# Kernel optimization log

Measured on AMD Instinct MI355X. Metric: run time of the kernel, lower is better.

The kernel has to match this reference:

```python
import jax, jax.numpy as jnp
import numpy as np

B = 16384      # batch
T = 14         # number of embedding tables
L = 100000     # rows per table (table has L+1 rows due to the +1 offset)
E = 16         # em_size
H = 50         # user click history length


def setup_inputs() -> dict:
    key = jax.random.key(0)
    ks = jax.random.split(key, 10)
    sparse_features = jax.random.randint(ks[0], (B, T), 0, L, dtype=jnp.int32)
    dense_features = jax.random.normal(ks[1], (B, 1), dtype=jnp.float32)
    user_click_history = jax.random.randint(ks[2], (B, H), 0, L, dtype=jnp.int32)
    # stacked EmbeddingBag weights: [T, L+1, E]
    W = jax.random.normal(ks[3], (T, L + 1, E), dtype=jnp.float32) * 0.01
    fc1_w = jax.random.normal(ks[4], (200, 241), dtype=jnp.float32) / np.sqrt(241).astype(np.float32)
    fc1_b = jnp.zeros((200,), jnp.float32)
    fc2_w = jax.random.normal(ks[5], (80, 200), dtype=jnp.float32) / np.sqrt(200).astype(np.float32)
    fc2_b = jnp.zeros((80,), jnp.float32)
    fc3_w = jax.random.normal(ks[6], (2, 80), dtype=jnp.float32) / np.sqrt(80).astype(np.float32)
    fc3_b = jnp.zeros((2,), jnp.float32)
    return dict(sparse_features=sparse_features, dense_features=dense_features,
                user_click_history=user_click_history, W=W,
                fc1_w=fc1_w, fc1_b=fc1_b, fc2_w=fc2_w, fc2_b=fc2_b,
                fc3_w=fc3_w, fc3_b=fc3_b)


def reference(sparse_features, dense_features, user_click_history, W,
              fc1_w, fc1_b, fc2_w, fc2_b, fc3_w, fc3_b):
    # Per-table single-index EmbeddingBag(sum) == plain lookup. Batched gather
    # across all T tables at once: [B, T, E]
    embs = W[jnp.arange(T)[None, :], sparse_features + 1]
    embs = embs.reshape(embs.shape[0], T * E)  # [B, T*E]
    # tables[0].weight row 0 is zeroed before the history lookup (padding row).
    W0 = W[0].at[0].set(0.0)
    hist = W0[user_click_history + 1].sum(axis=1)  # [B, E] EmbeddingBag sum
    x = jnp.concatenate([embs, hist, dense_features], axis=1)  # [B, 241]
    x = jax.nn.relu(x @ fc1_w.T + fc1_b)
    x = jax.nn.relu(x @ fc2_w.T + fc2_b)
    return x @ fc3_w.T + fc3_b  # [B, 2]
```

## Files before the change

### kernel.cpp

```cpp
#include <hip/hip_runtime.h>


using u16 = unsigned short;
typedef __attribute__((ext_vector_type(8))) short short8v;
typedef __attribute__((ext_vector_type(4))) float floatx4;

constexpr int BM = 32;
constexpr int NBLK = 16384 / BM;

constexpr int W1_ELEMS = 13 * 8 * 64 * 8;
constexpr int W2_ELEMS = 5 * 7 * 64 * 8;

__device__ __forceinline__ u16 f2bf(float f) {
  unsigned u = __float_as_uint(f);
  unsigned r = (u + 0x7fffu + ((u >> 16) & 1u)) >> 16;
  return (u16)r;
}
__device__ __forceinline__ float bf2f(u16 h) {
  return __uint_as_float(((unsigned)h) << 16);
}

__device__ __forceinline__ void wrA1(u16* Ah, u16* Al, int r, int k, float v) {
  u16 hi = f2bf(v);
  u16 lo = f2bf(v - bf2f(hi));
  int kt = k >> 5, kg = (k >> 3) & 3, e = k & 7;
  int lane = kg * 16 + (r & 15);
  int idx = (((r >> 4) * 8 + kt) * 64 + lane) * 8 + e;
  Ah[idx] = hi;
  Al[idx] = lo;
}

__global__ void build_frags(const float* __restrict__ w1, const float* __restrict__ w2,
                            u16* __restrict__ w1h, u16* __restrict__ w2h) {
  int tid = blockIdx.x * blockDim.x + threadIdx.x;
  if (tid < 13 * 8 * 64) {
    int l = tid & 63;
    int g = tid >> 6;
    int kt = g & 7, nt = g >> 3;
    int n = nt * 16 + (l & 15);
    int kb = kt * 32 + (l >> 4) * 8;
    short8v h8;
#pragma unroll
    for (int e = 0; e < 8; ++e) {
      int k = kb + e;
      float v = (n < 200 && k < 241) ? w1[n * 241 + k] : 0.f;
      h8[e] = (short)f2bf(v);
    }
    *(short8v*)&w1h[tid * 8] = h8;
  } else if (tid < 13 * 8 * 64 + 5 * 7 * 64) {
    int t2 = tid - 13 * 8 * 64;
    int l = t2 & 63;
    int g = t2 >> 6;
    int kt = g % 7, nt = g / 7;
    int n = nt * 16 + (l & 15);
    int kb = kt * 32 + (l >> 4) * 8;
    short8v h8;
#pragma unroll
    for (int e = 0; e < 8; ++e) {
      int k = kb + e;
      float v = (k < 200) ? w2[n * 200 + k] : 0.f;
      h8[e] = (short)f2bf(v);
    }
    *(short8v*)&w2h[t2 * 8] = h8;
  }
}

__global__ __launch_bounds__(1024, 8) void fused_kernel(
    const int* __restrict__ sf, const float* __restrict__ dense,
    const int* __restrict__ hist, const float* __restrict__ W,
    const u16* __restrict__ w1h, const u16* __restrict__ w2h,
    const float* __restrict__ b1, const float* __restrict__ b2,
    const float* __restrict__ w3, const float* __restrict__ b3,
    float* __restrict__ out) {
  __shared__ u16 sm[16384];
  __shared__ float psum[32 * 68];
  const int tid = threadIdx.x;
  const int row0 = blockIdx.x * BM;
  const int l = tid & 63;
  const int wv = tid >> 6;
  const int rh = wv & 1;
  const int pg = wv >> 1;

  short8v z8 = {0, 0, 0, 0, 0, 0, 0, 0};

  short8v bhr[2];
#pragma unroll
  for (int s = 0; s < 2; ++s) {
    int nt = pg + 8 * s;
    bhr[s] = (nt < 13) ? *(const short8v*)&w1h[((nt * 8 + 0) * 64 + l) * 8] : z8;
  }

#pragma unroll
  for (int i = 0; i < 2; ++i) *(short8v*)&sm[(tid + i * 1024) * 8] = z8;
  __syncthreads();

  u16* A1h = sm;
  u16* A1l = sm + 8192;

  if (tid < 512) {
    int r = tid >> 4, rem = tid & 15, q = rem >> 2, s = rem & 3;
    int rg = row0 + r;
    int beg = s * 12 + (s < 2 ? s : 2);
    int cnt = 12 + (s < 2 ? 1 : 0);
    float a0 = 0.f, a1 = 0.f, a2 = 0.f, a3 = 0.f;
    const int* hp = hist + rg * 50;
#pragma unroll 4
    for (int h = beg; h < beg + cnt; ++h) {
      int idx = hp[h] + 1;
      const float* p = W + (size_t)idx * 16 + q * 4;
      a0 += p[0];
      a1 += p[1];
      a2 += p[2];
      a3 += p[3];
    }
    float* ps = &psum[r * 68 + (q * 4) * 4 + s];
    ps[0] = a0;
    ps[4] = a1;
    ps[8] = a2;
    ps[12] = a3;
  } else {
    int tid2 = tid - 512;
#pragma unroll
    for (int it = 0; it < 4; ++it) {
      int g = tid2 + it * 512;
      if (g < 1792) {
        int q = g & 3, rt = g >> 2;
        int r = rt & 31, t = rt >> 5;
        int rg = row0 + r;
        int idx = sf[rg * 14 + t] + 1;
        const float* p = W + ((size_t)t * 100001 + (size_t)idx) * 16 + q * 4;
        float v0 = p[0], v1 = p[1], v2 = p[2], v3 = p[3];
        int kb = t * 16 + q * 4;
        wrA1(A1h, A1l, r, kb + 0, v0);
        wrA1(A1h, A1l, r, kb + 1, v1);
        wrA1(A1h, A1l, r, kb + 2, v2);
        wrA1(A1h, A1l, r, kb + 3, v3);
      }
    }
  }
  __syncthreads();

  if (tid < 512) {
    int r = tid >> 4, d = tid & 15;
    const float* ps = &psum[r * 68 + d * 4];
    float v = ps[0] + ps[1] + ps[2] + ps[3];
    wrA1(A1h, A1l, r, 224 + d, v);
    if (d == 0) wrA1(A1h, A1l, r, 240, dense[row0 + r]);
  }
  __syncthreads();

  floatx4 acc[2];
#pragma unroll
  for (int i = 0; i < 2; ++i) acc[i] = (floatx4){0.f, 0.f, 0.f, 0.f};

#pragma unroll
  for (int kt = 0; kt < 8; ++kt) {
    short8v ah = *(const short8v*)&A1h[((rh * 8 + kt) * 64 + l) * 8];
    short8v al = *(const short8v*)&A1l[((rh * 8 + kt) * 64 + l) * 8];
#pragma unroll
    for (int j = 0; j < 2; ++j) {
      int f = kt * 2 + j;
      int nt = pg + 8 * j;
      short8v cbh = bhr[j];
      int f2 = f + 2;
      if (f2 < 16) {
        int nt2 = pg + 8 * (f2 & 1);
        int kt2 = f2 >> 1;
        if (nt2 < 13) bhr[j] = *(const short8v*)&w1h[((nt2 * 8 + kt2) * 64 + l) * 8];
      }
      if (nt < 13) {
        acc[j] = __builtin_amdgcn_mfma_f32_16x16x32_bf16(ah, cbh, acc[j], 0, 0, 0);
        acc[j] = __builtin_amdgcn_mfma_f32_16x16x32_bf16(al, cbh, acc[j], 0, 0, 0);
      }
    }
  }
  __syncthreads();

#pragma unroll
  for (int i = 0; i < 2; ++i) {
    int b = tid + i * 1024;
    if (b < 1792) *(short8v*)&sm[b * 8] = z8;
  }
  __syncthreads();

  u16* A2h = sm;
  u16* A2l = sm + 7168;

#pragma unroll
  for (int j = 0; j < 2; ++j) {
    int nt = pg + 8 * j;
    if (nt < 13) {
      int n = nt * 16 + (l & 15);
      if (n < 200) {
        float bias = b1[n];
#pragma unroll
        for (int rg_ = 0; rg_ < 4; ++rg_) {
          float v = fmaxf(acc[j][rg_] + bias, 0.f);
          int m = (l >> 4) * 4 + rg_;
          u16 hi = f2bf(v);
          u16 lo = f2bf(v - bf2f(hi));
          int kt = n >> 5, kg = (n >> 3) & 3, e = n & 7;
          int lane2 = kg * 16 + m;
          int idx = ((rh * 7 + kt) * 64 + lane2) * 8 + e;
          A2h[idx] = hi;
          A2l[idx] = lo;
        }
      }
    }
  }
  __syncthreads();

  floatx4 acc2 = (floatx4){0.f, 0.f, 0.f, 0.f};
  if (pg < 5) {
    short8v b2hr[2];
    b2hr[0] = *(const short8v*)&w2h[((pg * 7 + 0) * 64 + l) * 8];
    b2hr[1] = *(const short8v*)&w2h[((pg * 7 + 1) * 64 + l) * 8];
#pragma unroll
    for (int kt = 0; kt < 7; ++kt) {
      short8v ah = *(const short8v*)&A2h[((rh * 7 + kt) * 64 + l) * 8];
      short8v al = *(const short8v*)&A2l[((rh * 7 + kt) * 64 + l) * 8];
      short8v cb = b2hr[kt & 1];
      if (kt + 2 < 7) b2hr[kt & 1] = *(const short8v*)&w2h[((pg * 7 + kt + 2) * 64 + l) * 8];
      acc2 = __builtin_amdgcn_mfma_f32_16x16x32_bf16(ah, cb, acc2, 0, 0, 0);
      acc2 = __builtin_amdgcn_mfma_f32_16x16x32_bf16(al, cb, acc2, 0, 0, 0);
    }
  }
  __syncthreads();

  float* o2 = (float*)sm;
  if (pg < 5) {
    int n = pg * 16 + (l & 15);
    float bias = b2[n];
#pragma unroll
    for (int rg_ = 0; rg_ < 4; ++rg_) {
      int r = rh * 16 + (l >> 4) * 4 + rg_;
      float v = fmaxf(acc2[rg_] + bias, 0.f);
      o2[r * 81 + n] = v;
    }
  }
  __syncthreads();

  if (tid < 64) {
    int r = tid >> 1, o = tid & 1;
    float a = b3[o];
#pragma unroll 8
    for (int j = 0; j < 80; ++j) a += o2[r * 81 + j] * w3[o * 80 + j];
    out[(row0 + r) * 2 + o] = a;
  }
}

extern "C" void kernel_launch(void* const* d_in, const int* in_sizes, int n_in,
                              void* d_out, int out_size, void* d_ws, size_t ws_size,
                              hipStream_t stream) {
  const int* sf = (const int*)d_in[0];
  const float* dense = (const float*)d_in[1];
  const int* hist = (const int*)d_in[2];
  const float* W = (const float*)d_in[3];
  const float* w1 = (const float*)d_in[4];
  const float* b1 = (const float*)d_in[5];
  const float* w2 = (const float*)d_in[6];
  const float* b2 = (const float*)d_in[7];
  const float* w3 = (const float*)d_in[8];
  const float* b3 = (const float*)d_in[9];
  float* out = (float*)d_out;

  u16* w1h = (u16*)d_ws;
  u16* w2h = w1h + W1_ELEMS;

  build_frags<<<dim3(35), dim3(256), 0, stream>>>(w1, w2, w1h, w2h);
  fused_kernel<<<dim3(NBLK), dim3(1024), 0, stream>>>(sf, dense, hist, W, w1h, w2h,
                                                      b1, b2, w3, b3, out);
}
```

Measured before the change: 30.92 us.

## Shrink blocks to 16 rows and 4 waves, redistribute MFMA tiles per wave

Each block now handles 16 batch rows with 256 threads instead of 32 rows with 1024 threads, launching 1024 blocks. Each wave now computes several fc1 and fc2 N-tiles rather than one or two. The history sum is reduced with lane shuffles instead of a shared-memory partial-sum pass, and embedding fragments are written as packed 4-element vectors. Several zero-fill passes and barriers are removed. The aim is better occupancy and latency hiding for the gather-heavy work and fewer synchronisations, at the cost of reloading the weight fragments for every 16 rows instead of every 32.

```diff
diff --git a/kernel.cpp b/kernel.cpp
--- a/kernel.cpp
+++ b/kernel.cpp
@@ -3,10 +3,8 @@
 
 using u16 = unsigned short;
 typedef __attribute__((ext_vector_type(8))) short short8v;
+typedef __attribute__((ext_vector_type(4))) short short4v;
 typedef __attribute__((ext_vector_type(4))) float floatx4;
-
-constexpr int BM = 32;
-constexpr int NBLK = 16384 / BM;
 
 constexpr int W1_ELEMS = 13 * 8 * 64 * 8;
 constexpr int W2_ELEMS = 5 * 7 * 64 * 8;
@@ -18,16 +16,6 @@
 }
 __device__ __forceinline__ float bf2f(u16 h) {
   return __uint_as_float(((unsigned)h) << 16);
-}
-
-__device__ __forceinline__ void wrA1(u16* Ah, u16* Al, int r, int k, float v) {
-  u16 hi = f2bf(v);
-  u16 lo = f2bf(v - bf2f(hi));
-  int kt = k >> 5, kg = (k >> 3) & 3, e = k & 7;
-  int lane = kg * 16 + (r & 15);
-  int idx = (((r >> 4) * 8 + kt) * 64 + lane) * 8 + e;
-  Ah[idx] = hi;
-  Al[idx] = lo;
 }
 
 __global__ void build_frags(const float* __restrict__ w1, const float* __restrict__ w2,
@@ -65,186 +53,218 @@
   }
 }
 
-__global__ __launch_bounds__(1024, 8) void fused_kernel(
+__global__ __launch_bounds__(256, 4) void fused_kernel(
     const int* __restrict__ sf, const float* __restrict__ dense,
     const int* __restrict__ hist, const float* __restrict__ W,
     const u16* __restrict__ w1h, const u16* __restrict__ w2h,
     const float* __restrict__ b1, const float* __restrict__ b2,
     const float* __restrict__ w3, const float* __restrict__ b3,
     float* __restrict__ out) {
-  __shared__ u16 sm[16384];
-  __shared__ float psum[32 * 68];
+  __shared__ u16 A1h[8 * 64 * 8], A1l[8 * 64 * 8];
+  __shared__ u16 A2h[7 * 64 * 8], A2l[7 * 64 * 8];
+  __shared__ float o2[16 * 84];
+
   const int tid = threadIdx.x;
-  const int row0 = blockIdx.x * BM;
   const int l = tid & 63;
   const int wv = tid >> 6;
-  const int rh = wv & 1;
-  const int pg = wv >> 1;
-
+  const int row0 = blockIdx.x * 16;
   short8v z8 = {0, 0, 0, 0, 0, 0, 0, 0};
 
-  short8v bhr[2];
-#pragma unroll
-  for (int s = 0; s < 2; ++s) {
-    int nt = pg + 8 * s;
-    bhr[s] = (nt < 13) ? *(const short8v*)&w1h[((nt * 8 + 0) * 64 + l) * 8] : z8;
-  }
-
-#pragma unroll
-  for (int i = 0; i < 2; ++i) *(short8v*)&sm[(tid + i * 1024) * 8] = z8;
-  __syncthreads();
-
-  u16* A1h = sm;
-  u16* A1l = sm + 8192;
-
-  if (tid < 512) {
-    int r = tid >> 4, rem = tid & 15, q = rem >> 2, s = rem & 3;
-    int rg = row0 + r;
-    int beg = s * 12 + (s < 2 ? s : 2);
-    int cnt = 12 + (s < 2 ? 1 : 0);
+  const int ntbase = (wv == 0) ? 0 : 4 + 3 * (wv - 1);
+  const int ntcnt = (wv == 0) ? 4 : 3;
+
+  short8v bhr[2][4];
+#pragma unroll
+  for (int kk = 0; kk < 2; ++kk)
+#pragma unroll
+    for (int i = 0; i < 4; ++i)
+      bhr[kk][i] = (i < ntcnt) ? *(const short8v*)&w1h[(((ntbase + i) * 8 + kk) * 64 + l) * 8]
+                               : z8;
+
+#pragma unroll
+  for (int it = 0; it < 4; ++it) {
+    int g = tid + it * 256;
+    if (g < 896) {
+      int q = g & 3, rt = g >> 2;
+      int r = rt & 15, t = rt >> 4;
+      int idx = sf[(row0 + r) * 14 + t] + 1;
+      const float* p = W + ((size_t)t * 100001 + (size_t)idx) * 16 + q * 4;
+      int k0 = t * 16 + q * 4;
+      int kt = k0 >> 5, kg = (k0 >> 3) & 3, e0 = k0 & 7;
+      short4v h4, l4;
+#pragma unroll
+      for (int d = 0; d < 4; ++d) {
+        float v = p[d];
+        u16 hi = f2bf(v);
+        h4[d] = (short)hi;
+        l4[d] = (short)f2bf(v - bf2f(hi));
+      }
+      int base = (kt * 64 + kg * 16 + r) * 8 + e0;
+      *(short4v*)&A1h[base] = h4;
+      *(short4v*)&A1l[base] = l4;
+    }
+  }
+
+  {
+    int r = tid >> 4, rem = tid & 15, q = rem & 3, s = rem >> 2;
+    const int* hp = hist + (row0 + r) * 50;
+    const float* Wq = W + q * 4;
     float a0 = 0.f, a1 = 0.f, a2 = 0.f, a3 = 0.f;
-    const int* hp = hist + rg * 50;
-#pragma unroll 4
-    for (int h = beg; h < beg + cnt; ++h) {
-      int idx = hp[h] + 1;
-      const float* p = W + (size_t)idx * 16 + q * 4;
+#pragma unroll
+    for (int hh = 0; hh < 12; ++hh) {
+      int idx = hp[s + hh * 4] + 1;
+      const float* p = Wq + (size_t)idx * 16;
       a0 += p[0];
       a1 += p[1];
       a2 += p[2];
       a3 += p[3];
     }
-    float* ps = &psum[r * 68 + (q * 4) * 4 + s];
-    ps[0] = a0;
-    ps[4] = a1;
-    ps[8] = a2;
-    ps[12] = a3;
+    if (s < 2) {
+      int idx = hp[48 + s] + 1;
+      const float* p = Wq + (size_t)idx * 16;
+      a0 += p[0];
+      a1 += p[1];
+      a2 += p[2];
+      a3 += p[3];
+    }
+    a0 += __shfl_xor(a0, 4);
+    a1 += __shfl_xor(a1, 4);
+    a2 += __shfl_xor(a2, 4);
+    a3 += __shfl_xor(a3, 4);
+    a0 += __shfl_xor(a0, 8);
+    a1 += __shfl_xor(a1, 8);
+    a2 += __shfl_xor(a2, 8);
+    a3 += __shfl_xor(a3, 8);
+    if (s == 0) {
+      float vals[4] = {a0, a1, a2, a3};
+      short4v h4, l4;
+#pragma unroll
+      for (int d = 0; d < 4; ++d) {
+        u16 hi = f2bf(vals[d]);
+        h4[d] = (short)hi;
+        l4[d] = (short)f2bf(vals[d] - bf2f(hi));
+      }
+      int base = (7 * 64 + (q >> 1) * 16 + r) * 8 + ((q * 4) & 7);
+      *(short4v*)&A1h[base] = h4;
+      *(short4v*)&A1l[base] = l4;
+      if (q == 0) {
+        float dv = dense[row0 + r];
+        u16 dh = f2bf(dv), dl = f2bf(dv - bf2f(dh));
+        short8v dh8 = z8, dl8 = z8;
+        dh8[0] = (short)dh;
+        dl8[0] = (short)dl;
+        *(short8v*)&A1h[(7 * 64 + 32 + r) * 8] = dh8;
+        *(short8v*)&A1l[(7 * 64 + 32 + r) * 8] = dl8;
+        *(short8v*)&A1h[(7 * 64 + 48 + r) * 8] = z8;
+        *(short8v*)&A1l[(7 * 64 + 48 + r) * 8] = z8;
+      }
+    }
+  }
+  __syncthreads();
+
+  floatx4 acc[4];
+#pragma unroll
+  for (int i = 0; i < 4; ++i) acc[i] = (floatx4){0.f, 0.f, 0.f, 0.f};
+
+#pragma unroll
+  for (int kt = 0; kt < 8; ++kt) {
+    short8v ah = *(const short8v*)&A1h[(kt * 64 + l) * 8];
+    short8v al = *(const short8v*)&A1l[(kt * 64 + l) * 8];
+#pragma unroll
+    for (int i = 0; i < 4; ++i) {
+      if (i < ntcnt) {
+        short8v cb = bhr[kt & 1][i];
+        if (kt < 6) bhr[kt & 1][i] = *(const short8v*)&w1h[(((ntbase + i) * 8 + kt + 2) * 64 + l) * 8];
+        acc[i] = __builtin_amdgcn_mfma_f32_16x16x32_bf16(ah, cb, acc[i], 0, 0, 0);
+        acc[i] = __builtin_amdgcn_mfma_f32_16x16x32_bf16(al, cb, acc[i], 0, 0, 0);
+      }
+    }
+  }
+
+  const int ntA = wv;
+  short8v bra[2], brb[2];
+  bra[0] = *(const short8v*)&w2h[((ntA * 7 + 0) * 64 + l) * 8];
+  bra[1] = *(const short8v*)&w2h[((ntA * 7 + 1) * 64 + l) * 8];
+  if (wv == 0) {
+    brb[0] = *(const short8v*)&w2h[((4 * 7 + 0) * 64 + l) * 8];
+    brb[1] = *(const short8v*)&w2h[((4 * 7 + 1) * 64 + l) * 8];
   } else {
-    int tid2 = tid - 512;
-#pragma unroll
-    for (int it = 0; it < 4; ++it) {
-      int g = tid2 + it * 512;
-      if (g < 1792) {
-        int q = g & 3, rt = g >> 2;
-        int r = rt & 31, t = rt >> 5;
-        int rg = row0 + r;
-        int idx = sf[rg * 14 + t] + 1;
-        const float* p = W + ((size_t)t * 100001 + (size_t)idx) * 16 + q * 4;
-        float v0 = p[0], v1 = p[1], v2 = p[2], v3 = p[3];
-        int kb = t * 16 + q * 4;
-        wrA1(A1h, A1l, r, kb + 0, v0);
-        wrA1(A1h, A1l, r, kb + 1, v1);
-        wrA1(A1h, A1l, r, kb + 2, v2);
-        wrA1(A1h, A1l, r, kb + 3, v3);
-      }
-    }
+    brb[0] = z8;
+    brb[1] = z8;
+  }
+
+#pragma unroll
+  for (int i = 0; i < 4; ++i) {
+    if (i < ntcnt) {
+      int n = (ntbase + i) * 16 + (l & 15);
+      float bias = (n < 200) ? b1[n] : 0.f;
+#pragma unroll
+      for (int g = 0; g < 4; ++g) {
+        float v = (n < 200) ? fmaxf(acc[i][g] + bias, 0.f) : 0.f;
+        int m = (l >> 4) * 4 + g;
+        u16 hi = f2bf(v), lo = f2bf(v - bf2f(hi));
+        int kt2 = n >> 5, kg2 = (n >> 3) & 3, e = n & 7;
+        int pos = (kt2 * 64 + kg2 * 16 + m) * 8 + e;
+        A2h[pos] = hi;
+        A2l[pos] = lo;
+      }
+    }
+  }
+  if (wv == 1 && l < 32) {
+    *(short8v*)&A2h[(6 * 64 + 32 + l) * 8] = z8;
+    *(short8v*)&A2l[(6 * 64 + 32 + l) * 8] = z8;
   }
   __syncthreads();
 
-  if (tid < 512) {
-    int r = tid >> 4, d = tid & 15;
-    const float* ps = &psum[r * 68 + d * 4];
-    float v = ps[0] + ps[1] + ps[2] + ps[3];
-    wrA1(A1h, A1l, r, 224 + d, v);
-    if (d == 0) wrA1(A1h, A1l, r, 240, dense[row0 + r]);
+  floatx4 acca = (floatx4){0.f, 0.f, 0.f, 0.f};
+  floatx4 accb = (floatx4){0.f, 0.f, 0.f, 0.f};
+#pragma unroll
+  for (int kt = 0; kt < 7; ++kt) {
+    short8v ah = *(const short8v*)&A2h[(kt * 64 + l) * 8];
+    short8v al = *(const short8v*)&A2l[(kt * 64 + l) * 8];
+    short8v ca = bra[kt & 1];
+    if (kt < 5) bra[kt & 1] = *(const short8v*)&w2h[((ntA * 7 + kt + 2) * 64 + l) * 8];
+    acca = __builtin_amdgcn_mfma_f32_16x16x32_bf16(ah, ca, acca, 0, 0, 0);
+    acca = __builtin_amdgcn_mfma_f32_16x16x32_bf16(al, ca, acca, 0, 0, 0);
+    if (wv == 0) {
+      short8v cb = brb[kt & 1];
+      if (kt < 5) brb[kt & 1] = *(const short8v*)&w2h[((4 * 7 + kt + 2) * 64 + l) * 8];
+      accb = __builtin_amdgcn_mfma_f32_16x16x32_bf16(ah, cb, accb, 0, 0, 0);
+      accb = __builtin_amdgcn_mfma_f32_16x16x32_bf16(al, cb, accb, 0, 0, 0);
+    }
+  }
+
+  {
+    int n = ntA * 16 + (l & 15);
+    float bias = b2[n];
+#pragma unroll
+    for (int g = 0; g < 4; ++g) {
+      int r = (l >> 4) * 4 + g;
+      o2[r * 84 + n] = fmaxf(acca[g] + bias, 0.f);
+    }
+    if (wv == 0) {
+      int n2 = 64 + (l & 15);
+      float bias2 = b2[n2];
+#pragma unroll
+      for (int g = 0; g < 4; ++g) {
+        int r = (l >> 4) * 4 + g;
+        o2[r * 84 + n2] = fmaxf(accb[g] + bias2, 0.f);
+      }
+    }
   }
   __syncthreads();
 
-  floatx4 acc[2];
-#pragma unroll
-  for (int i = 0; i < 2; ++i) acc[i] = (floatx4){0.f, 0.f, 0.f, 0.f};
-
-#pragma unroll
-  for (int kt = 0; kt < 8; ++kt) {
-    short8v ah = *(const short8v*)&A1h[((rh * 8 + kt) * 64 + l) * 8];
-    short8v al = *(const short8v*)&A1l[((rh * 8 + kt) * 64 + l) * 8];
-#pragma unroll
-    for (int j = 0; j < 2; ++j) {
-      int f = kt * 2 + j;
-      int nt = pg + 8 * j;
-      short8v cbh = bhr[j];
-      int f2 = f + 2;
-      if (f2 < 16) {
-        int nt2 = pg + 8 * (f2 & 1);
-        int kt2 = f2 >> 1;
-        if (nt2 < 13) bhr[j] = *(const short8v*)&w1h[((nt2 * 8 + kt2) * 64 + l) * 8];
-      }
-      if (nt < 13) {
-        acc[j] = __builtin_amdgcn_mfma_f32_16x16x32_bf16(ah, cbh, acc[j], 0, 0, 0);
-        acc[j] = __builtin_amdgcn_mfma_f32_16x16x32_bf16(al, cbh, acc[j], 0, 0, 0);
-      }
-    }
-  }
-  __syncthreads();
-
-#pragma unroll
-  for (int i = 0; i < 2; ++i) {
-    int b = tid + i * 1024;
-    if (b < 1792) *(short8v*)&sm[b * 8] = z8;
-  }
-  __syncthreads();
-
-  u16* A2h = sm;
-  u16* A2l = sm + 7168;
-
-#pragma unroll
-  for (int j = 0; j < 2; ++j) {
-    int nt = pg + 8 * j;
-    if (nt < 13) {
-      int n = nt * 16 + (l & 15);
-      if (n < 200) {
-        float bias = b1[n];
-#pragma unroll
-        for (int rg_ = 0; rg_ < 4; ++rg_) {
-          float v = fmaxf(acc[j][rg_] + bias, 0.f);
-          int m = (l >> 4) * 4 + rg_;
-          u16 hi = f2bf(v);
-          u16 lo = f2bf(v - bf2f(hi));
-          int kt = n >> 5, kg = (n >> 3) & 3, e = n & 7;
-          int lane2 = kg * 16 + m;
-          int idx = ((rh * 7 + kt) * 64 + lane2) * 8 + e;
-          A2h[idx] = hi;
-          A2l[idx] = lo;
-        }
-      }
-    }
-  }
-  __syncthreads();
-
-  floatx4 acc2 = (floatx4){0.f, 0.f, 0.f, 0.f};
-  if (pg < 5) {
-    short8v b2hr[2];
-    b2hr[0] = *(const short8v*)&w2h[((pg * 7 + 0) * 64 + l) * 8];
-    b2hr[1] = *(const short8v*)&w2h[((pg * 7 + 1) * 64 + l) * 8];
-#pragma unroll
-    for (int kt = 0; kt < 7; ++kt) {
-      short8v ah = *(const short8v*)&A2h[((rh * 7 + kt) * 64 + l) * 8];
-      short8v al = *(const short8v*)&A2l[((rh * 7 + kt) * 64 + l) * 8];
-      short8v cb = b2hr[kt & 1];
-      if (kt + 2 < 7) b2hr[kt & 1] = *(const short8v*)&w2h[((pg * 7 + kt + 2) * 64 + l) * 8];
-      acc2 = __builtin_amdgcn_mfma_f32_16x16x32_bf16(ah, cb, acc2, 0, 0, 0);
-      acc2 = __builtin_amdgcn_mfma_f32_16x16x32_bf16(al, cb, acc2, 0, 0, 0);
-    }
-  }
-  __syncthreads();
-
-  float* o2 = (float*)sm;
-  if (pg < 5) {
-    int n = pg * 16 + (l & 15);
-    float bias = b2[n];
-#pragma unroll
-    for (int rg_ = 0; rg_ < 4; ++rg_) {
-      int r = rh * 16 + (l >> 4) * 4 + rg_;
-      float v = fmaxf(acc2[rg_] + bias, 0.f);
-      o2[r * 81 + n] = v;
-    }
-  }
-  __syncthreads();
-
-  if (tid < 64) {
+  if (tid < 32) {
     int r = tid >> 1, o = tid & 1;
     float a = b3[o];
-#pragma unroll 8
-    for (int j = 0; j < 80; ++j) a += o2[r * 81 + j] * w3[o * 80 + j];
+    const float* orow = &o2[r * 84];
+    const float* wrow = &w3[o * 80];
+#pragma unroll
+    for (int j = 0; j < 80; j += 4) {
+      floatx4 xv = *(const floatx4*)&orow[j];
+      floatx4 wv4 = *(const floatx4*)&wrow[j];
+      a += xv[0] * wv4[0] + xv[1] * wv4[1] + xv[2] * wv4[2] + xv[3] * wv4[3];
+    }
     out[(row0 + r) * 2 + o] = a;
   }
 }
@@ -268,6 +288,6 @@
   u16* w2h = w1h + W1_ELEMS;
 
   build_frags<<<dim3(35), dim3(256), 0, stream>>>(w1, w2, w1h, w2h);
-  fused_kernel<<<dim3(NBLK), dim3(1024), 0, stream>>>(sf, dense, hist, W, w1h, w2h,
-                                                      b1, b2, w3, b3, out);
-}
+  fused_kernel<<<dim3(1024), dim3(256), 0, stream>>>(sf, dense, hist, W, w1h, w2h,
+                                                     b1, b2, w3, b3, out);
+}
```

Result: no change. 31.08 us (+0.5%).
